# Kernel tuning notes

Hardware: AMD Instinct MI355X
Metric: run time of the kernel (lower is better)

## Reference

```python
import jax, jax.numpy as jnp
import numpy as np

BS, SEQ, H = 64, 512, 768
E, T, K = 32, 64, 64


def setup_inputs() -> dict:
    key = jax.random.key(0)
    ks = jax.random.split(key, 16)
    return {
        "hidden_states": jax.random.normal(ks[0], (BS, SEQ, H), dtype=jnp.float32),
        "Wsrc": jax.random.normal(ks[1], (862, 384), dtype=jnp.float32) * 0.02,
        "Wtgt": jax.random.normal(ks[2], (862, 384), dtype=jnp.float32) * 0.02,
        "W_cls": jax.random.normal(ks[3], (2, 6144), dtype=jnp.float32) * 0.02,
        "b_cls": jnp.zeros((2,), dtype=jnp.float32),
        "W_topic": jax.random.normal(ks[4], (2, 6144), dtype=jnp.float32) * 0.02,
        "b_topic": jnp.zeros((2,), dtype=jnp.float32),
        "W_token": jax.random.normal(ks[5], (2, 6144), dtype=jnp.float32) * 0.02,
        "b_token": jnp.zeros((2,), dtype=jnp.float32),
        "source_ids": jax.random.randint(ks[6], (BS,), 0, 862),
        "target_ids": jax.random.randint(ks[7], (BS,), 0, 862),
        "ent_inds": jax.random.randint(ks[8], (BS, E), 0, SEQ - 1),
        "ent_mask": jnp.ones((BS, E), dtype=jnp.float32),
        "topic_inds": jax.random.randint(ks[9], (BS, T), 0, SEQ),
        "topic_mask": jnp.ones((BS, T), dtype=jnp.float32),
        "token_inds": jax.random.randint(ks[10], (BS, K), 0, SEQ),
        "token_mask": jnp.ones((BS, K), dtype=jnp.float32),
    }


def reference(hidden_states, Wsrc, Wtgt, W_cls, b_cls, W_topic, b_topic,
              W_token, b_token, source_ids, target_ids, ent_inds, ent_mask,
              topic_inds, topic_mask, token_inds, token_mask):
    bs = hidden_states.shape[0]
    # domain embedding: concat(source_emb, target_emb) -> [bs, 768] -> [bs, 96, 8]
    domain = jnp.concatenate([Wsrc[source_ids], Wtgt[target_ids]], axis=1)
    d0 = domain.reshape(bs, 96, 8)

    def gather(inds, mask, offset=0):
        # ragged gather of hidden states at token positions, zero-padded slots masked
        h = jnp.take_along_axis(hidden_states, (inds + offset)[:, :, None], axis=1)
        return h * mask[:, :, None]  # [bs, L, 768]

    ent_h = gather(ent_inds, ent_mask, offset=1)
    topic_h = gather(topic_inds, topic_mask)
    token_h = gather(token_inds, token_mask)

    # CLS bilinear: outer product over the 8-dim factor, [bs,96,8,8] -> [bs,6144]
    cls_h = hidden_states[:, 0, :].reshape(bs, 96, 8)
    bl_cls = (d0[:, :, :, None] * cls_h[:, :, None, :]).reshape(bs, 6144)
    cls_logits = jax.nn.softmax(bl_cls @ W_cls.T + b_cls, axis=1)

    def bilin(h, W, b):
        h4 = h.reshape(bs, -1, 96, 8)  # [bs, L, 96, 8]
        bl = (d0[:, None, :, :, None] * h4[:, :, :, None, :]).reshape(bs, h4.shape[1], 6144)
        return bl @ W.T + b  # [bs, L, n_out]

    topic_logits = jax.nn.softmax(bilin(topic_h, W_topic, b_topic), axis=2)
    token_logits = bilin(token_h, W_token, b_token)
    return cls_logits, topic_logits, token_logits
```

## Files before the change

kernel.cpp:

```cpp
#include <hip/hip_runtime.h>

#define BSZ 64
#define SEQ 512
#define HD  768
#define TT  64
#define NPART 8
#define TPP 16

__global__ __launch_bounds__(256) void fused_kernel(
    const float* __restrict__ hidden,
    const float* __restrict__ Wsrc,
    const float* __restrict__ Wtgt,
    const float* __restrict__ W_cls,
    const float* __restrict__ W_topic,
    const float* __restrict__ W_token,
    const float* __restrict__ b_cls,
    const float* __restrict__ b_topic,
    const float* __restrict__ b_token,
    const int*   __restrict__ source_ids,
    const int*   __restrict__ target_ids,
    const int*   __restrict__ topic_inds,
    const float* __restrict__ topic_mask,
    const int*   __restrict__ token_inds,
    const float* __restrict__ token_mask,
    float*       __restrict__ out)
{
    __shared__ __align__(16) float dom[HD];
    __shared__ __align__(16) float Vl[4][HD];

    const int blk = blockIdx.x;
    const int b   = blk >> 3;
    const int p   = blk & 7;
    const int tid = threadIdx.x;

    const int sid = source_ids[b];
    const int tgt = target_ids[b];
    for (int j = tid; j < HD; j += 256)
        dom[j] = (j < 384) ? Wsrc[sid * 384 + j] : Wtgt[tgt * 384 + (j - 384)];
    __syncthreads();

    int base_row, nrows;
    if (p == 0)      { base_row = 0; nrows = 4; }
    else if (p < 4)  { base_row = 2; nrows = 2; }
    else             { base_row = 4; nrows = 2; }

    for (int idx = tid; idx < nrows * HD; idx += 256) {
        const int ri = idx / HD;
        const int d  = idx - ri * HD;
        const int r  = base_row + ri;
        const int w  = r >> 1, o = r & 1;
        const float* Wp = (w == 0) ? W_cls : (w == 1) ? W_topic : W_token;
        const int m = d >> 3, c = d & 7;
        const float* wrow = Wp + o * 6144 + m * 64 + c;
        float acc = 0.f;
        #pragma unroll
        for (int a = 0; a < 8; ++a)
            acc = fmaf(dom[m * 8 + a], wrow[a * 8], acc);
        Vl[ri][d] = acc;
    }
    __syncthreads();

    const int wid  = tid >> 6;
    const int lane = tid & 63;
    const int ntasks = (p == 0) ? (1 + TPP) : TPP;

    for (int ti = wid; ti < ntasks; ti += 4) {
        int pos, outoff, vbase;
        float mask;
        const float* bias;
        bool do_softmax;
        if (p == 0 && ti == 0) {
            pos = 0; mask = 1.f; bias = b_cls; do_softmax = true;
            outoff = b * 2; vbase = 0;
        } else if (p < 4) {
            const int l = (p == 0) ? (ti - 1) : (p * TPP + ti);
            pos = topic_inds[b * TT + l]; mask = topic_mask[b * TT + l];
            bias = b_topic; do_softmax = true;
            outoff = 128 + (b * TT + l) * 2;
            vbase = (p == 0) ? 2 : 0;
        } else {
            const int l = (p - 4) * TPP + ti;
            pos = token_inds[b * TT + l]; mask = token_mask[b * TT + l];
            bias = b_token; do_softmax = false;
            outoff = 128 + BSZ * TT * 2 + (b * TT + l) * 2;
            vbase = 0;
        }

        const float4* hrow = reinterpret_cast<const float4*>(
            hidden + ((size_t)b * SEQ + (size_t)pos) * HD);
        const float4* v0 = reinterpret_cast<const float4*>(&Vl[vbase][0]);
        const float4* v1 = reinterpret_cast<const float4*>(&Vl[vbase + 1][0]);

        float a0 = 0.f, a1 = 0.f;
        #pragma unroll
        for (int k = 0; k < 3; ++k) {
            const float4 h4 = hrow[lane + k * 64];
            const float4 x0 = v0[lane + k * 64];
            const float4 x1 = v1[lane + k * 64];
            a0 = fmaf(h4.x, x0.x, a0); a1 = fmaf(h4.x, x1.x, a1);
            a0 = fmaf(h4.y, x0.y, a0); a1 = fmaf(h4.y, x1.y, a1);
            a0 = fmaf(h4.z, x0.z, a0); a1 = fmaf(h4.z, x1.z, a1);
            a0 = fmaf(h4.w, x0.w, a0); a1 = fmaf(h4.w, x1.w, a1);
        }
        #pragma unroll
        for (int off = 32; off > 0; off >>= 1) {
            a0 += __shfl_down(a0, off, 64);
            a1 += __shfl_down(a1, off, 64);
        }

        if (lane == 0) {
            const float l0 = fmaf(mask, a0, bias[0]);
            const float l1 = fmaf(mask, a1, bias[1]);
            if (do_softmax) {
                const float mx = fmaxf(l0, l1);
                const float e0 = __expf(l0 - mx);
                const float e1 = __expf(l1 - mx);
                const float inv = 1.f / (e0 + e1);
                out[outoff]     = e0 * inv;
                out[outoff + 1] = e1 * inv;
            } else {
                out[outoff]     = l0;
                out[outoff + 1] = l1;
            }
        }
    }
}

extern "C" void kernel_launch(void* const* d_in, const int* in_sizes, int n_in,
                              void* d_out, int out_size, void* d_ws, size_t ws_size,
                              hipStream_t stream) {
    const float* hidden     = (const float*)d_in[0];
    const float* Wsrc       = (const float*)d_in[1];
    const float* Wtgt       = (const float*)d_in[2];
    const float* W_cls      = (const float*)d_in[3];
    const float* b_cls      = (const float*)d_in[4];
    const float* W_topic    = (const float*)d_in[5];
    const float* b_topic    = (const float*)d_in[6];
    const float* W_token    = (const float*)d_in[7];
    const float* b_token    = (const float*)d_in[8];
    const int*   source_ids = (const int*)d_in[9];
    const int*   target_ids = (const int*)d_in[10];
    const int*   topic_inds = (const int*)d_in[13];
    const float* topic_mask = (const float*)d_in[14];
    const int*   token_inds = (const int*)d_in[15];
    const float* token_mask = (const float*)d_in[16];
    float* out = (float*)d_out;

    fused_kernel<<<BSZ * NPART, 256, 0, stream>>>(
        hidden, Wsrc, Wtgt, W_cls, W_topic, W_token,
        b_cls, b_topic, b_token, source_ids, target_ids,
        topic_inds, topic_mask, token_inds, token_mask, out);
}
```

Measured before the change: 165.9 us.

## Split work into 33 blocks per batch, one row per wavefront

```diff
diff --git a/kernel.cpp b/kernel.cpp
--- a/kernel.cpp
+++ b/kernel.cpp
@@ -4,8 +4,7 @@
 #define SEQ 512
 #define HD  768
 #define TT  64
-#define NPART 8
-#define TPP 16
+#define BPB 33
 
 __global__ __launch_bounds__(256) void fused_kernel(
     const float* __restrict__ hidden,
@@ -26,11 +25,11 @@
     float*       __restrict__ out)
 {
     __shared__ __align__(16) float dom[HD];
-    __shared__ __align__(16) float Vl[4][HD];
+    __shared__ __align__(16) float Vl[2][HD];
 
     const int blk = blockIdx.x;
-    const int b   = blk >> 3;
-    const int p   = blk & 7;
+    const int b   = blk / BPB;
+    const int q   = blk - b * BPB;
     const int tid = threadIdx.x;
 
     const int sid = source_ids[b];
@@ -39,57 +38,50 @@
         dom[j] = (j < 384) ? Wsrc[sid * 384 + j] : Wtgt[tgt * 384 + (j - 384)];
     __syncthreads();
 
-    int base_row, nrows;
-    if (p == 0)      { base_row = 0; nrows = 4; }
-    else if (p < 4)  { base_row = 2; nrows = 2; }
-    else             { base_row = 4; nrows = 2; }
-
-    for (int idx = tid; idx < nrows * HD; idx += 256) {
-        const int ri = idx / HD;
-        const int d  = idx - ri * HD;
-        const int r  = base_row + ri;
-        const int w  = r >> 1, o = r & 1;
-        const float* Wp = (w == 0) ? W_cls : (w == 1) ? W_topic : W_token;
+    const float* Wp = (q == 0) ? W_cls : (q <= 16) ? W_topic : W_token;
+    for (int idx = tid; idx < 2 * HD; idx += 256) {
+        const int o = (idx >= HD) ? 1 : 0;
+        const int d = idx - o * HD;
         const int m = d >> 3, c = d & 7;
         const float* wrow = Wp + o * 6144 + m * 64 + c;
         float acc = 0.f;
         #pragma unroll
         for (int a = 0; a < 8; ++a)
             acc = fmaf(dom[m * 8 + a], wrow[a * 8], acc);
-        Vl[ri][d] = acc;
+        Vl[o][d] = acc;
     }
     __syncthreads();
 
     const int wid  = tid >> 6;
     const int lane = tid & 63;
-    const int ntasks = (p == 0) ? (1 + TPP) : TPP;
 
-    for (int ti = wid; ti < ntasks; ti += 4) {
-        int pos, outoff, vbase;
-        float mask;
-        const float* bias;
-        bool do_softmax;
-        if (p == 0 && ti == 0) {
-            pos = 0; mask = 1.f; bias = b_cls; do_softmax = true;
-            outoff = b * 2; vbase = 0;
-        } else if (p < 4) {
-            const int l = (p == 0) ? (ti - 1) : (p * TPP + ti);
-            pos = topic_inds[b * TT + l]; mask = topic_mask[b * TT + l];
-            bias = b_topic; do_softmax = true;
-            outoff = 128 + (b * TT + l) * 2;
-            vbase = (p == 0) ? 2 : 0;
-        } else {
-            const int l = (p - 4) * TPP + ti;
-            pos = token_inds[b * TT + l]; mask = token_mask[b * TT + l];
-            bias = b_token; do_softmax = false;
-            outoff = 128 + BSZ * TT * 2 + (b * TT + l) * 2;
-            vbase = 0;
-        }
+    int pos, outoff;
+    float mask;
+    const float* bias;
+    bool do_softmax;
+    bool active = true;
 
+    if (q == 0) {
+        active = (wid == 0);
+        pos = 0; mask = 1.f; bias = b_cls; do_softmax = true;
+        outoff = b * 2;
+    } else if (q <= 16) {
+        const int l = (q - 1) * 4 + wid;
+        pos = topic_inds[b * TT + l]; mask = topic_mask[b * TT + l];
+        bias = b_topic; do_softmax = true;
+        outoff = 128 + (b * TT + l) * 2;
+    } else {
+        const int l = (q - 17) * 4 + wid;
+        pos = token_inds[b * TT + l]; mask = token_mask[b * TT + l];
+        bias = b_token; do_softmax = false;
+        outoff = 128 + BSZ * TT * 2 + (b * TT + l) * 2;
+    }
+
+    if (active) {
         const float4* hrow = reinterpret_cast<const float4*>(
             hidden + ((size_t)b * SEQ + (size_t)pos) * HD);
-        const float4* v0 = reinterpret_cast<const float4*>(&Vl[vbase][0]);
-        const float4* v1 = reinterpret_cast<const float4*>(&Vl[vbase + 1][0]);
+        const float4* v0 = reinterpret_cast<const float4*>(&Vl[0][0]);
+        const float4* v1 = reinterpret_cast<const float4*>(&Vl[1][0]);
 
         float a0 = 0.f, a1 = 0.f;
         #pragma unroll
@@ -146,7 +138,7 @@
     const float* token_mask = (const float*)d_in[16];
     float* out = (float*)d_out;
 
-    fused_kernel<<<BSZ * NPART, 256, 0, stream>>>(
+    fused_kernel<<<BSZ * BPB, 256, 0, stream>>>(
         hidden, Wsrc, Wtgt, W_cls, W_topic, W_token,
         b_cls, b_topic, b_token, source_ids, target_ids,
         topic_inds, topic_mask, token_inds, token_mask, out);
```

New measurement: 166.0 us. Within noise of the previous version (+0.0%).
